# Kernel tuning notes

Hardware: AMD Instinct MI355X
Metric: run time of the kernel (lower is better)

## Reference

```python
import jax, jax.numpy as jnp
import numpy as np

N = 50000      # nodes
E = 500000     # edges
G = 8          # graphs in batch
IN = 128       # in_dim
HID = 64       # hidden_dim_graph == hidden_dim1
H = 2          # num_heads
C = 2          # n_classes
SLOPE = 0.2    # DGL GATConv leaky_relu negative slope


def setup_inputs() -> dict:
    key = jax.random.key(0)
    ks = jax.random.split(key, 16)
    s = lambda k, sh, fan: (jax.random.normal(k, sh, jnp.float32) / np.float32(np.sqrt(fan)))
    return {
        "h_n": jax.random.normal(ks[0], (N, IN), jnp.float32),
        "src": jax.random.randint(ks[1], (E,), 0, N),
        "dst": jax.random.randint(ks[2], (E,), 0, N),
        "graph_ids": jnp.sort(jax.random.randint(ks[3], (N,), 0, G)),
        # GATConv layer 1: fc [IN, H*HID], attn vectors [H, HID]
        "W_fc1": s(ks[4], (IN, H * HID), IN),
        "attn_l1": s(ks[5], (H, HID), HID),
        "attn_r1": s(ks[6], (H, HID), HID),
        # GATConv layer 2: fc [HID, H*HID]
        "W_fc2": s(ks[7], (HID, H * HID), HID),
        "attn_l2": s(ks[8], (H, HID), HID),
        "attn_r2": s(ks[9], (H, HID), HID),
        # gate nn: Linear(HID, 1)
        "w_gate": s(ks[10], (HID, 1), HID),
        "b_gate": jnp.zeros((1,), jnp.float32),
        # classifier MLP
        "W_c1": s(ks[11], (HID, HID), HID),
        "b_c1": jnp.zeros((HID,), jnp.float32),
        "W_c2": s(ks[12], (HID, C), HID),
        "b_c2": jnp.zeros((C,), jnp.float32),
    }


def _gat_conv(h, src, dst, W_fc, attn_l, attn_r):
    # h: [N, D_in] -> out: [N, H, HID]
    feat = (h @ W_fc).reshape(N, H, HID)
    el = (feat * attn_l).sum(-1)                 # [N, H]
    er = (feat * attn_r).sum(-1)                 # [N, H]
    e = jax.nn.leaky_relu(el[src] + er[dst], SLOPE)   # [E, H]
    # edge softmax over incoming edges per destination node
    m = jax.ops.segment_max(e, dst, num_segments=N)   # [N, H]
    ex = jnp.exp(e - m[dst])                     # [E, H]
    den = jax.ops.segment_sum(ex, dst, num_segments=N)
    alpha = ex / jnp.where(den == 0, 1.0, den)[dst]
    # message passing: sum_e alpha_e * feat[src_e]
    return jax.ops.segment_sum(alpha[:, :, None] * feat[src], dst, num_segments=N)


def _segment_softmax(x, ids, num_segments):
    m = jax.ops.segment_max(x, ids, num_segments=num_segments)
    ex = jnp.exp(x - m[ids])
    den = jax.ops.segment_sum(ex, ids, num_segments=num_segments)
    return ex / jnp.where(den == 0, 1.0, den)[ids]


def reference(h_n, src, dst, graph_ids, W_fc1, attn_l1, attn_r1, W_fc2, attn_l2,
              attn_r2, w_gate, b_gate, W_c1, b_c1, W_c2, b_c2):
    h = jax.nn.relu(_gat_conv(h_n, src, dst, W_fc1, attn_l1, attn_r1)).mean(axis=1)
    h = jax.nn.relu(_gat_conv(h, src, dst, W_fc2, attn_l2, attn_r2)).mean(axis=1)
    # global attention pooling (gate MLP + per-graph softmax + weighted sum)
    gate = (h @ w_gate + b_gate)[:, 0]                 # [N]
    a = _segment_softmax(gate, graph_ids, G)[:, None]  # [N, 1]
    hg = jax.ops.segment_sum(a * h, graph_ids, num_segments=G)  # [G, HID]
    # classifier head (dropout is identity in eval mode)
    a2 = hg @ W_c1 + b_c1
    a3 = a2 @ W_c2 + b_c2
    return (jax.nn.sigmoid(a3), a, hg)
```

## Files before the change

kernel.cpp:

```cpp
#include <hip/hip_runtime.h>
#include <hip/hip_bf16.h>

#define NN 50000
#define EE 500000
#define GG 8
#define INDIM 128
#define HID 64
#define NH 2
#define PB 32
#define TM 32
#define KC 32
#define CAP 64
#define NB_SC ((EE + 255) / 256)

__device__ inline unsigned short f2bf(float f) {
    unsigned int u = __float_as_uint(f);
    unsigned int r = (u + 0x7FFFu + ((u >> 16) & 1u)) >> 16;
    return (unsigned short)r;
}
__device__ inline unsigned int pack_bf16x2(float lo, float hi) {
    return (unsigned int)f2bf(lo) | ((unsigned int)f2bf(hi) << 16);
}
__device__ inline unsigned int encf(float f) {
    unsigned int u = __float_as_uint(f);
    return (u & 0x80000000u) ? ~u : (u | 0x80000000u);
}
__device__ inline float decf(unsigned int e) {
    unsigned int u = (e & 0x80000000u) ? (e & 0x7FFFFFFFu) : ~e;
    return __uint_as_float(u);
}
__device__ inline int lower_bound_g(const int* __restrict__ gids, int target, int N) {
    int lo = 0, hi = N;
    while (lo < hi) { int mid = (lo + hi) >> 1; if (gids[mid] < target) lo = mid + 1; else hi = mid; }
    return lo;
}

__device__ __forceinline__ void fc_attn_body(
        int bid, const float* __restrict__ X, const float* __restrict__ W,
        const float* __restrict__ al, const float* __restrict__ ar,
        unsigned int* __restrict__ featb, float* __restrict__ el,
        float* __restrict__ er, int K, int N) {
    int t = threadIdx.x;
    int tx = t & 31, ty = t >> 5;
    int n0 = bid * TM;
    __shared__ float xT[KC][TM + 4];
    __shared__ float Wsh[KC][128];
    float acc[4][4] = {{0.f}};

    for (int kc = 0; kc < K; kc += KC) {
        {
            int r = t >> 3;
            int c4 = (t & 7) * 4;
            int n = n0 + r;
            float4 v = make_float4(0.f, 0.f, 0.f, 0.f);
            if (n < N) v = *(const float4*)&X[(size_t)n * K + kc + c4];
            xT[c4 + 0][r] = v.x;
            xT[c4 + 1][r] = v.y;
            xT[c4 + 2][r] = v.z;
            xT[c4 + 3][r] = v.w;
        }
        {
            const float4* Wg = (const float4*)&W[(size_t)kc * 128];
            float4* Ws4 = (float4*)&Wsh[0][0];
#pragma unroll
            for (int i = 0; i < 4; i++) Ws4[t + 256 * i] = Wg[t + 256 * i];
        }
        __syncthreads();
#pragma unroll
        for (int k = 0; k < KC; k++) {
            float4 xv = *(float4*)&xT[k][ty * 4];
            float4 wv = *(float4*)&Wsh[k][tx * 4];
            float xs[4] = {xv.x, xv.y, xv.z, xv.w};
            float wsv[4] = {wv.x, wv.y, wv.z, wv.w};
#pragma unroll
            for (int i = 0; i < 4; i++)
#pragma unroll
                for (int j = 0; j < 4; j++) acc[i][j] += xs[i] * wsv[j];
        }
        __syncthreads();
    }

    int head = tx >> 4;
    float alv[4], arv[4];
#pragma unroll
    for (int j = 0; j < 4; j++) {
        alv[j] = al[tx * 4 + j];
        arv[j] = ar[tx * 4 + j];
    }
#pragma unroll
    for (int i = 0; i < 4; i++) {
        int r = n0 + ty * 4 + i;
        if (r < N) {
            uint2 pk;
            pk.x = pack_bf16x2(acc[i][0], acc[i][1]);
            pk.y = pack_bf16x2(acc[i][2], acc[i][3]);
            *(uint2*)&featb[(size_t)r * 64 + tx * 2] = pk;
            float pl = 0.f, pr = 0.f;
#pragma unroll
            for (int j = 0; j < 4; j++) {
                pl += acc[i][j] * alv[j];
                pr += acc[i][j] * arv[j];
            }
            for (int off = 8; off; off >>= 1) {
                pl += __shfl_xor(pl, off, 64);
                pr += __shfl_xor(pr, off, 64);
            }
            if ((tx & 15) == 0) {
                el[r * 2 + head] = pl;
                er[r * 2 + head] = pr;
            }
        }
    }
}

__global__ __launch_bounds__(256) void build_fc1_kernel(
        const int* __restrict__ src, const int* __restrict__ dst,
        int* __restrict__ cnt, unsigned short* __restrict__ esrc,
        const float* __restrict__ X, const float* __restrict__ W,
        const float* __restrict__ al, const float* __restrict__ ar,
        unsigned int* __restrict__ featb, float* __restrict__ el,
        float* __restrict__ er) {
    if (blockIdx.x < NB_SC) {
        int e = blockIdx.x * 256 + threadIdx.x;
        if (e < EE) {
            int d = dst[e];
            int pos = atomicAdd(&cnt[d], 1);
            if (pos < CAP) esrc[(size_t)d * CAP + pos] = (unsigned short)src[e];
        }
        return;
    }
    fc_attn_body(blockIdx.x - NB_SC, X, W, al, ar, featb, el, er, 128, NN);
}

__global__ __launch_bounds__(256) void fc_attn_kernel(
        const float* __restrict__ X, const float* __restrict__ W,
        const float* __restrict__ al, const float* __restrict__ ar,
        unsigned int* __restrict__ featb, float* __restrict__ el,
        float* __restrict__ er, int K, int N) {
    fc_attn_body(blockIdx.x, X, W, al, ar, featb, el, er, K, N);
}

__global__ void gat_agg_kernel(const unsigned int* __restrict__ featb,
                               const float* __restrict__ el,
                               const float* __restrict__ er, const int* __restrict__ cnt,
                               const unsigned short* __restrict__ esrc,
                               float* __restrict__ hout,
                               const float* __restrict__ wg, const float* __restrict__ bg,
                               float* __restrict__ gatev, int doGate) {
    int wid = threadIdx.x >> 6;
    int lane = threadIdx.x & 63;
    int n = blockIdx.x * 4 + wid;
    if (n >= NN) return;
    int deg = cnt[n];
    deg = deg > CAP ? CAP : deg;
    int q = lane >> 4;
    int l4 = lane & 15;
    float a8[8];
#pragma unroll
    for (int i = 0; i < 8; i++) a8[i] = 0.f;

    if (deg > 0) {
        float2 erv = ((const float2*)er)[n];
        bool v = lane < deg;
        int s = (int)esrc[(size_t)n * CAP + (v ? lane : 0)];
        float2 elv = ((const float2*)el)[s];
        float e0 = elv.x + erv.x; e0 = e0 > 0.f ? e0 : 0.2f * e0;
        float e1 = elv.y + erv.y; e1 = e1 > 0.f ? e1 : 0.2f * e1;
        float x0 = v ? __expf(e0) : 0.f;
        float x1 = v ? __expf(e1) : 0.f;
        float d0 = x0, d1 = x1;
        for (int off = 32; off; off >>= 1) {
            d0 += __shfl_xor(d0, off, 64);
            d1 += __shfl_xor(d1, off, 64);
        }
        float a0 = x0 / d0, a1 = x1 / d1;
        int headHi = (l4 >= 8);
        for (int e = 0; e < deg; e += 4) {
            int myE = e + q;
            bool ve = myE < deg;
            int pick = ve ? myE : e;
            int se = __shfl(s, pick, 64);
            float av0 = __shfl(a0, pick, 64);
            float av1 = __shfl(a1, pick, 64);
            float a = headHi ? av1 : av0;
            if (!ve) a = 0.f;
            uint4 fv = *(const uint4*)&featb[(size_t)se * 64 + l4 * 4];
            a8[0] += a * __uint_as_float(fv.x << 16);
            a8[1] += a * __uint_as_float(fv.x & 0xFFFF0000u);
            a8[2] += a * __uint_as_float(fv.y << 16);
            a8[3] += a * __uint_as_float(fv.y & 0xFFFF0000u);
            a8[4] += a * __uint_as_float(fv.z << 16);
            a8[5] += a * __uint_as_float(fv.z & 0xFFFF0000u);
            a8[6] += a * __uint_as_float(fv.w << 16);
            a8[7] += a * __uint_as_float(fv.w & 0xFFFF0000u);
        }
    }

#pragma unroll
    for (int i = 0; i < 8; i++) {
        a8[i] += __shfl_xor(a8[i], 16, 64);
        a8[i] += __shfl_xor(a8[i], 32, 64);
        a8[i] = fmaxf(a8[i], 0.f);
    }
    float m8[8];
#pragma unroll
    for (int i = 0; i < 8; i++) m8[i] = 0.5f * (a8[i] + __shfl_xor(a8[i], 8, 64));
    if (lane < 8) {
        float4 w0 = make_float4(m8[0], m8[1], m8[2], m8[3]);
        float4 w1 = make_float4(m8[4], m8[5], m8[6], m8[7]);
        *(float4*)&hout[(size_t)n * 64 + 8 * lane] = w0;
        *(float4*)&hout[(size_t)n * 64 + 8 * lane + 4] = w1;
    }

    if (doGate) {
        float val = 0.f;
        if (lane < 8) {
#pragma unroll
            for (int i = 0; i < 8; i++) val += m8[i] * wg[8 * lane + i];
        }
        val += __shfl_xor(val, 1, 64);
        val += __shfl_xor(val, 2, 64);
        val += __shfl_xor(val, 4, 64);
        if (lane == 0) gatev[n] = val + bg[0];
    }
}

__global__ void pool_max_kernel(const float* __restrict__ gatev, const int* __restrict__ gids,
                                unsigned int* __restrict__ gmEnc) {
    int g = blockIdx.x / PB, b = blockIdx.x % PB;
    __shared__ int sb[2];
    int t = threadIdx.x;
    if (t == 0) { sb[0] = lower_bound_g(gids, g, NN); sb[1] = lower_bound_g(gids, g + 1, NN); }
    __syncthreads();
    int lo = sb[0], len = sb[1] - lo;
    int s = lo + (int)((long long)b * len / PB);
    int e = lo + (int)((long long)(b + 1) * len / PB);
    float m = -3.4e38f;
    for (int n = s + t; n < e; n += 256) m = fmaxf(m, gatev[n]);
    __shared__ float red[4];
    int w = t >> 6, lane = t & 63;
    for (int off = 32; off; off >>= 1) m = fmaxf(m, __shfl_down(m, off, 64));
    if (lane == 0) red[w] = m;
    __syncthreads();
    if (t == 0) {
        m = fmaxf(fmaxf(red[0], red[1]), fmaxf(red[2], red[3]));
        atomicMax(&gmEnc[g], encf(m));
    }
}

__global__ void pool_expacc_kernel(const float* __restrict__ h2, const float* __restrict__ gatev,
                                   const int* __restrict__ gids,
                                   const unsigned int* __restrict__ gmEnc,
                                   float* __restrict__ out_a, float* __restrict__ gsum,
                                   float* __restrict__ hgacc) {
    int g = blockIdx.x / PB, b = blockIdx.x % PB;
    __shared__ int sb[2];
    int t = threadIdx.x;
    if (t == 0) { sb[0] = lower_bound_g(gids, g, NN); sb[1] = lower_bound_g(gids, g + 1, NN); }
    __syncthreads();
    int lo = sb[0], len = sb[1] - lo;
    int s = lo + (int)((long long)b * len / PB);
    int e = lo + (int)((long long)(b + 1) * len / PB);
    float m = decf(gmEnc[g]);
    int sub = t >> 6, c = t & 63;
    float acc = 0.f, esum = 0.f;
    for (int n = s + sub; n < e; n += 4) {
        float ev = __expf(gatev[n] - m);
        if (c == 0) out_a[n] = ev;
        esum += ev;
        acc += ev * h2[(size_t)n * 64 + c];
    }
    __shared__ float sh[4][64];
    sh[sub][c] = acc;
    __syncthreads();
    if (sub == 0) atomicAdd(&hgacc[g * 64 + c], sh[0][c] + sh[1][c] + sh[2][c] + sh[3][c]);
    if (c == 0) atomicAdd(&gsum[g], esum);
}

__global__ __launch_bounds__(512) void epilogue_kernel(
        const float* __restrict__ hgacc, const float* __restrict__ gsum,
        const float* __restrict__ Wc1, const float* __restrict__ bc1,
        const float* __restrict__ Wc2, const float* __restrict__ bc2,
        const int* __restrict__ gids, float* __restrict__ out,
        float* __restrict__ out_a, float* __restrict__ out_hg) {
    int t = threadIdx.x;
    if (blockIdx.x != 0) {
        int n = (blockIdx.x - 1) * 512 + t;
        if (n < NN) {
            float sv = gsum[gids[n]];
            out_a[n] *= (sv > 0.f) ? 1.f / sv : 0.f;
        }
        return;
    }
    __shared__ float hgs[GG * 64];
    __shared__ float a2s[GG * 64];
    int g = t >> 6, c = t & 63;
    float sv = gsum[g];
    float inv = (sv > 0.f) ? 1.f / sv : 0.f;
    float hval = hgacc[t] * inv;
    hgs[t] = hval;
    out_hg[t] = hval;
    __syncthreads();
    float acc = bc1[c];
    for (int k = 0; k < 64; k++) acc += hgs[g * 64 + k] * Wc1[k * 64 + c];
    a2s[g * 64 + c] = acc;
    __syncthreads();
    if (t < GG * 2) {
        int gg = t >> 1, j = t & 1;
        float a3 = bc2[j];
        for (int k = 0; k < 64; k++) a3 += a2s[gg * 64 + k] * Wc2[k * 2 + j];
        out[t] = 1.f / (1.f + expf(-a3));
    }
}

extern "C" void kernel_launch(void* const* d_in, const int* in_sizes, int n_in,
                              void* d_out, int out_size, void* d_ws, size_t ws_size,
                              hipStream_t stream) {
    const float* h_n  = (const float*)d_in[0];
    const int*   src  = (const int*)d_in[1];
    const int*   dst  = (const int*)d_in[2];
    const int*   gids = (const int*)d_in[3];
    const float* Wfc1 = (const float*)d_in[4];
    const float* al1  = (const float*)d_in[5];
    const float* ar1  = (const float*)d_in[6];
    const float* Wfc2 = (const float*)d_in[7];
    const float* al2  = (const float*)d_in[8];
    const float* ar2  = (const float*)d_in[9];
    const float* wg   = (const float*)d_in[10];
    const float* bg   = (const float*)d_in[11];
    const float* Wc1  = (const float*)d_in[12];
    const float* bc1  = (const float*)d_in[13];
    const float* Wc2  = (const float*)d_in[14];
    const float* bc2  = (const float*)d_in[15];
    float* out = (float*)d_out;

    float* ws     = (float*)d_ws;
    unsigned int* featb = (unsigned int*)ws;
    float* el     = ws + (size_t)NN * 64;
    float* er     = el + NN * 2;
    float* hbuf   = er + NN * 2;
    float* gatev  = hbuf + (size_t)NN * 64;
    unsigned int* gmEnc = (unsigned int*)(gatev + NN);
    float* gsum   = (float*)(gmEnc + GG);
    float* hgacc  = gsum + GG;
    int*   cnt    = (int*)(hgacc + GG * 64);
    unsigned short* esrc = (unsigned short*)(cnt + NN);

    size_t zero_bytes = (GG + GG + GG * 64 + NN) * 4;
    hipMemsetAsync(gmEnc, 0, zero_bytes, stream);

    int nb1 = NB_SC + (NN + TM - 1) / TM;
    build_fc1_kernel<<<nb1, 256, 0, stream>>>(src, dst, cnt, esrc,
                                              h_n, Wfc1, al1, ar1, featb, el, er);
    gat_agg_kernel<<<(NN + 3) / 4, 256, 0, stream>>>(featb, el, er, cnt, esrc, hbuf,
                                                     wg, bg, gatev, 0);

    fc_attn_kernel<<<(NN + TM - 1) / TM, 256, 0, stream>>>(hbuf, Wfc2, al2, ar2,
                                                           featb, el, er, 64, NN);
    gat_agg_kernel<<<(NN + 3) / 4, 256, 0, stream>>>(featb, el, er, cnt, esrc, hbuf,
                                                     wg, bg, gatev, 1);

    pool_max_kernel<<<GG * PB, 256, 0, stream>>>(gatev, gids, gmEnc);
    pool_expacc_kernel<<<GG * PB, 256, 0, stream>>>(hbuf, gatev, gids, gmEnc,
                                                    out + GG * 2, gsum, hgacc);

    int nb = 1 + (NN + 511) / 512;
    epilogue_kernel<<<nb, 512, 0, stream>>>(hgacc, gsum, Wc1, bc1, Wc2, bc2, gids,
                                            out, out + GG * 2, out + GG * 2 + NN);
}
```

Baseline: 272.5 us.

## Replace FP32 FC tile GEMM with bf16 MFMA and swizzled LDS staging

The node-feature linear layers now convert X and W to bf16 in swizzled shared memory and compute 64-row tiles with 16x16x32 bf16 MFMA instructions instead of scalar FP32 FMAs on 32-row tiles. Output is staged through LDS so rows can be written to global memory as coalesced 16-byte stores. The attention dot products el/er are then computed from the bf16-rounded staged features. This cuts ALU time in the FC stages. In exchange, inputs are rounded to bf16 before multiplication, which adds numeric error, and the 48 KB shared buffer may lower occupancy, including for the fused scatter blocks.

```diff
diff --git a/kernel.cpp b/kernel.cpp
--- a/kernel.cpp
+++ b/kernel.cpp
@@ -8,10 +8,13 @@
 #define HID 64
 #define NH 2
 #define PB 32
-#define TM 32
-#define KC 32
+#define TMM 64
 #define CAP 64
 #define NB_SC ((EE + 255) / 256)
+
+typedef __bf16 bf16x4 __attribute__((ext_vector_type(4)));
+typedef __bf16 bf16x8 __attribute__((ext_vector_type(8)));
+typedef float  f32x4  __attribute__((ext_vector_type(4)));
 
 __device__ inline unsigned short f2bf(float f) {
     unsigned int u = __float_as_uint(f);
@@ -35,80 +38,130 @@
     return lo;
 }
 
-__device__ __forceinline__ void fc_attn_body(
+__device__ __forceinline__ void fc_mfma_body(
         int bid, const float* __restrict__ X, const float* __restrict__ W,
         const float* __restrict__ al, const float* __restrict__ ar,
         unsigned int* __restrict__ featb, float* __restrict__ el,
         float* __restrict__ er, int K, int N) {
+    __shared__ __align__(16) char smem[49152];
+    char* Xb = smem;
+    char* Wb = smem + 16384;
+    char* Dt = smem;
+
     int t = threadIdx.x;
-    int tx = t & 31, ty = t >> 5;
-    int n0 = bid * TM;
-    __shared__ float xT[KC][TM + 4];
-    __shared__ float Wsh[KC][128];
-    float acc[4][4] = {{0.f}};
-
-    for (int kc = 0; kc < K; kc += KC) {
-        {
-            int r = t >> 3;
-            int c4 = (t & 7) * 4;
-            int n = n0 + r;
-            float4 v = make_float4(0.f, 0.f, 0.f, 0.f);
-            if (n < N) v = *(const float4*)&X[(size_t)n * K + kc + c4];
-            xT[c4 + 0][r] = v.x;
-            xT[c4 + 1][r] = v.y;
-            xT[c4 + 2][r] = v.z;
-            xT[c4 + 3][r] = v.w;
-        }
-        {
-            const float4* Wg = (const float4*)&W[(size_t)kc * 128];
-            float4* Ws4 = (float4*)&Wsh[0][0];
-#pragma unroll
-            for (int i = 0; i < 4; i++) Ws4[t + 256 * i] = Wg[t + 256 * i];
-        }
-        __syncthreads();
-#pragma unroll
-        for (int k = 0; k < KC; k++) {
-            float4 xv = *(float4*)&xT[k][ty * 4];
-            float4 wv = *(float4*)&Wsh[k][tx * 4];
-            float xs[4] = {xv.x, xv.y, xv.z, xv.w};
-            float wsv[4] = {wv.x, wv.y, wv.z, wv.w};
-#pragma unroll
-            for (int i = 0; i < 4; i++)
-#pragma unroll
-                for (int j = 0; j < 4; j++) acc[i][j] += xs[i] * wsv[j];
-        }
-        __syncthreads();
-    }
-
-    int head = tx >> 4;
-    float alv[4], arv[4];
-#pragma unroll
-    for (int j = 0; j < 4; j++) {
-        alv[j] = al[tx * 4 + j];
-        arv[j] = ar[tx * 4 + j];
-    }
-#pragma unroll
-    for (int i = 0; i < 4; i++) {
-        int r = n0 + ty * 4 + i;
-        if (r < N) {
-            uint2 pk;
-            pk.x = pack_bf16x2(acc[i][0], acc[i][1]);
-            pk.y = pack_bf16x2(acc[i][2], acc[i][3]);
-            *(uint2*)&featb[(size_t)r * 64 + tx * 2] = pk;
-            float pl = 0.f, pr = 0.f;
+    int n0 = bid * TMM;
+    int K2 = K * 2;
+    int k4sh = (K == 128) ? 5 : 4;
+    int K4m = (K >> 2) - 1;
+
+    for (int i = t; i < (TMM << k4sh); i += 256) {
+        int row = i >> k4sh, c4 = i & K4m;
+        int gr = n0 + row;
+        float4 v = make_float4(0.f, 0.f, 0.f, 0.f);
+        if (gr < N) v = *(const float4*)&X[(size_t)gr * K + (c4 << 2)];
+        int slot = c4 ^ (row & 7);
+        *(uint2*)(Xb + row * K2 + slot * 8) =
+            make_uint2(pack_bf16x2(v.x, v.y), pack_bf16x2(v.z, v.w));
+    }
+    for (int i = t; i < K * 32; i += 256) {
+        int k = i >> 5, c4 = (i & 31) << 2;
+        float4 v = *(const float4*)&W[(size_t)k * 128 + c4];
+        float fv[4] = {v.x, v.y, v.z, v.w};
+        int ksl = k >> 2, kb = (k & 3) * 2;
+#pragma unroll
+        for (int j = 0; j < 4; j++) {
+            int col = c4 + j;
+            *(unsigned short*)(Wb + col * K2 + ((ksl ^ (col & 7)) * 8) + kb) = f2bf(fv[j]);
+        }
+    }
+    __syncthreads();
+
+    int wv = t >> 6, l = t & 63;
+    int lr = l & 15, g = l >> 4;
+    f32x4 acc[4][2];
+#pragma unroll
+    for (int rb = 0; rb < 4; rb++)
+#pragma unroll
+        for (int cb = 0; cb < 2; cb++) acc[rb][cb] = (f32x4){0.f, 0.f, 0.f, 0.f};
+
+    int nks = K >> 5;
+    for (int ks = 0; ks < nks; ks++) {
+        bf16x8 af[4], bfr[2];
+#pragma unroll
+        for (int rb = 0; rb < 4; rb++) {
+            int r = rb * 16 + lr;
+            const char* base = Xb + r * K2;
+            int s0 = (ks * 8 + g) ^ (r & 7);
+            int s1 = (ks * 8 + g + 4) ^ (r & 7);
+            bf16x4 a0 = *(const bf16x4*)(base + s0 * 8);
+            bf16x4 a1 = *(const bf16x4*)(base + s1 * 8);
+            af[rb] = __builtin_shufflevector(a0, a1, 0, 1, 2, 3, 4, 5, 6, 7);
+        }
+#pragma unroll
+        for (int cb = 0; cb < 2; cb++) {
+            int c = wv * 32 + cb * 16 + lr;
+            const char* base = Wb + c * K2;
+            int s0 = (ks * 8 + g) ^ (c & 7);
+            int s1 = (ks * 8 + g + 4) ^ (c & 7);
+            bf16x4 b0 = *(const bf16x4*)(base + s0 * 8);
+            bf16x4 b1 = *(const bf16x4*)(base + s1 * 8);
+            bfr[cb] = __builtin_shufflevector(b0, b1, 0, 1, 2, 3, 4, 5, 6, 7);
+        }
+#pragma unroll
+        for (int rb = 0; rb < 4; rb++)
+#pragma unroll
+            for (int cb = 0; cb < 2; cb++)
+                acc[rb][cb] = __builtin_amdgcn_mfma_f32_16x16x32_bf16(
+                    af[rb], bfr[cb], acc[rb][cb], 0, 0, 0);
+    }
+    __syncthreads();
+
+#pragma unroll
+    for (int rb = 0; rb < 4; rb++)
+#pragma unroll
+        for (int cb = 0; cb < 2; cb++)
 #pragma unroll
             for (int j = 0; j < 4; j++) {
-                pl += acc[i][j] * alv[j];
-                pr += acc[i][j] * arv[j];
+                int row = rb * 16 + 4 * g + j;
+                int col = wv * 32 + cb * 16 + lr;
+                int byte = (col * 2) ^ ((row & 7) << 4);
+                *(unsigned short*)(Dt + row * 256 + byte) = f2bf(acc[rb][cb][j]);
             }
-            for (int off = 8; off; off >>= 1) {
-                pl += __shfl_xor(pl, off, 64);
-                pr += __shfl_xor(pr, off, 64);
+    __syncthreads();
+
+    for (int i = t; i < TMM * 16; i += 256) {
+        int row = i >> 4, s16 = i & 15;
+        uint4 v = *(const uint4*)(Dt + row * 256 + ((s16 * 16) ^ ((row & 7) << 4)));
+        int gr = n0 + row;
+        if (gr < N) *(uint4*)&featb[(size_t)gr * 64 + s16 * 4] = v;
+    }
+
+    {
+        int r = t >> 2, p = t & 3;
+        int h = p >> 1;
+        const float* alh = al + h * 64 + (p & 1) * 32;
+        const float* arh = ar + h * 64 + (p & 1) * 32;
+        float pl = 0.f, pr = 0.f;
+#pragma unroll
+        for (int ii = 0; ii < 4; ii++) {
+            int s16 = p * 4 + ii;
+            uint4 v = *(const uint4*)(Dt + r * 256 + ((s16 * 16) ^ ((r & 7) << 4)));
+            unsigned int uu[4] = {v.x, v.y, v.z, v.w};
+#pragma unroll
+            for (int q = 0; q < 4; q++) {
+                float flo = __uint_as_float(uu[q] << 16);
+                float fhi = __uint_as_float(uu[q] & 0xFFFF0000u);
+                int cb = ii * 8 + q * 2;
+                pl += flo * alh[cb] + fhi * alh[cb + 1];
+                pr += flo * arh[cb] + fhi * arh[cb + 1];
             }
-            if ((tx & 15) == 0) {
-                el[r * 2 + head] = pl;
-                er[r * 2 + head] = pr;
-            }
+        }
+        pl += __shfl_xor(pl, 1, 64);
+        pr += __shfl_xor(pr, 1, 64);
+        int gr = n0 + r;
+        if ((p & 1) == 0 && gr < N) {
+            el[gr * 2 + h] = pl;
+            er[gr * 2 + h] = pr;
         }
     }
 }
@@ -129,7 +182,7 @@
         }
         return;
     }
-    fc_attn_body(blockIdx.x - NB_SC, X, W, al, ar, featb, el, er, 128, NN);
+    fc_mfma_body(blockIdx.x - NB_SC, X, W, al, ar, featb, el, er, 128, NN);
 }
 
 __global__ __launch_bounds__(256) void fc_attn_kernel(
@@ -137,7 +190,7 @@
         const float* __restrict__ al, const float* __restrict__ ar,
         unsigned int* __restrict__ featb, float* __restrict__ el,
         float* __restrict__ er, int K, int N) {
-    fc_attn_body(blockIdx.x, X, W, al, ar, featb, el, er, K, N);
+    fc_mfma_body(blockIdx.x, X, W, al, ar, featb, el, er, K, N);
 }
 
 __global__ void gat_agg_kernel(const unsigned int* __restrict__ featb,
@@ -349,14 +402,14 @@
     size_t zero_bytes = (GG + GG + GG * 64 + NN) * 4;
     hipMemsetAsync(gmEnc, 0, zero_bytes, stream);
 
-    int nb1 = NB_SC + (NN + TM - 1) / TM;
-    build_fc1_kernel<<<nb1, 256, 0, stream>>>(src, dst, cnt, esrc,
-                                              h_n, Wfc1, al1, ar1, featb, el, er);
+    int nbFc1 = (NN + TMM - 1) / TMM;
+    build_fc1_kernel<<<NB_SC + nbFc1, 256, 0, stream>>>(src, dst, cnt, esrc,
+                                                        h_n, Wfc1, al1, ar1, featb, el, er);
     gat_agg_kernel<<<(NN + 3) / 4, 256, 0, stream>>>(featb, el, er, cnt, esrc, hbuf,
                                                      wg, bg, gatev, 0);
 
-    fc_attn_kernel<<<(NN + TM - 1) / TM, 256, 0, stream>>>(hbuf, Wfc2, al2, ar2,
-                                                           featb, el, er, 64, NN);
+    fc_attn_kernel<<<nbFc1, 256, 0, stream>>>(hbuf, Wfc2, al2, ar2,
+                                              featb, el, er, 64, NN);
     gat_agg_kernel<<<(NN + 3) / 4, 256, 0, stream>>>(featb, el, er, cnt, esrc, hbuf,
                                                      wg, bg, gatev, 1);
 
```

Result: slower. 284.7 us (+4.5%).
